# Kernel tuning notes

Hardware: AMD Instinct MI355X
Metric: run time of the kernel (lower is better)

The kernel has to match this reference:

```python
import jax, jax.numpy as jnp
import numpy as np
from jax import lax

B, L, D = 4, 2048, 1024
M = D // 4            # StructuredStateRecurrence memory_dim = dim//4
E, TOPK = 4, 2        # EnhancedGatedFusion defaults
H = D // 4            # LowRankFF hidden = dim//reduction_factor(4)
K, DIL = 5, 1         # SerriformBlock kernel_size=5, dilation init arg
EPS = 1e-6


def _rms(v, w):
    return w * v * lax.rsqrt(jnp.mean(v * v, axis=-1, keepdims=True) + EPS)


def setup_inputs() -> dict:
    key = jax.random.key(0)
    ks = jax.random.split(key, 16)
    g = lambda i, shape, s=0.02: jax.random.normal(ks[i], shape, jnp.float32) * s
    return {
        "x": jax.random.normal(ks[0], (B, L, D), jnp.float32),
        "memory_state": jnp.zeros((B, M), jnp.float32),
        "norm_w": jnp.ones((D,), jnp.float32),
        "dw_w": g(1, (D, K), 0.1),            # depthwise Conv1d weight [D,1,K] squeezed
        "dw_b": jnp.zeros((D,), jnp.float32),
        "pw_w": g(2, (D, D)),                 # pointwise Conv1d weight [D,D,1] squeezed
        "pw_b": jnp.zeros((D,), jnp.float32),
        "val_w": g(3, (M, D)),
        "val_b": jnp.zeros((M,), jnp.float32),
        "time_decay": g(4, (M,), 0.01),
        "time_first": g(5, (M,), 0.01),
        "gate_w": g(6, (D, D + M)),
        "gate_b": jnp.zeros((D,), jnp.float32),
        "router_w": g(7, (E, D)),
        "router_b": jnp.zeros((E,), jnp.float32),
        "exp_w": g(8, (E, D, D)),             # per-expert Linear(dim,dim) weights [out,in]
        "exp_b": jnp.zeros((E, D), jnp.float32),
        "out_w": g(9, (D, D)),
        "out_b": jnp.zeros((D,), jnp.float32),
        "fnorm_w": jnp.ones((D,), jnp.float32),
        "down_w": g(10, (H, D)),
        "down_b": jnp.zeros((H,), jnp.float32),
        "up_w": g(11, (D, H)),
        "up_b": jnp.zeros((D,), jnp.float32),
        "res_scale": jnp.array([0.9], jnp.float32),
    }


def reference(x, memory_state, norm_w, dw_w, dw_b, pw_w, pw_b, val_w, val_b,
              time_decay, time_first, gate_w, gate_b, router_w, router_b,
              exp_w, exp_b, out_w, out_b, fnorm_w, down_w, down_b, up_w,
              up_b, res_scale):
    h = _rms(x, norm_w)

    # --- FusedDWPWConv: causal depthwise conv + pointwise conv + SiLU ---
    pad = (K - 1) * DIL                                      # left causal pad (torch pads both, slices [:L])
    xc = jnp.swapaxes(h, 1, 2)                               # [B, D, L]
    y = lax.conv_general_dilated(xc, dw_w[:, None, :], (1,), [(pad, 0)],
                                 rhs_dilation=(DIL,),
                                 dimension_numbers=("NCL", "OIL", "NCL"),
                                 feature_group_count=D)
    y = y + dw_b[None, :, None]
    y = jax.nn.silu(jnp.einsum("oi,bil->bol", pw_w, y) + pw_b[None, :, None])
    h = jnp.swapaxes(y, 1, 2)                                # [B, L, D]

    # --- StructuredStateRecurrence: w[i] = decay*w[i-1] + v[i] (== torch's decay-mask sum) ---
    v = h @ val_w.T + val_b                                  # [B, L, M]
    decay = jax.nn.sigmoid(time_decay) * 0.9 + 0.1
    tfirst = jax.nn.sigmoid(time_first)

    def step(carry, v_t):
        w = carry * decay + v_t
        return w, w

    _, wv = lax.scan(step, jnp.zeros((x.shape[0], M), x.dtype), jnp.swapaxes(v, 0, 1))
    wv = jnp.swapaxes(wv, 0, 1)                              # [B, L, M]
    wv = wv + memory_state[:, None, :] * tfirst
    next_mem = wv[:, -1]
    h = h + jnp.concatenate([h, wv], axis=-1) @ gate_w.T + gate_b

    # --- EnhancedGatedFusion: top-k MoE over 4 experts ---
    logits = h @ router_w.T + router_b                       # [B, L, E]
    tk_logits, tk_idx = lax.top_k(logits, TOPK)
    tk_w = jax.nn.softmax(tk_logits, axis=-1)
    gates = jnp.sum(tk_w[..., None] * jax.nn.one_hot(tk_idx, E, dtype=h.dtype), axis=-2)  # [B,L,E]
    exp_out = jax.nn.silu(jnp.einsum("bli,eoi->bleo", h, exp_w) + exp_b)  # [B,L,E,D]
    comb = jnp.einsum("ble,bled->bld", gates, exp_out)
    h = _rms(h + comb @ out_w.T + out_b, fnorm_w)

    # --- LowRankFF (exact GELU, as torch nn.GELU default) ---
    ff = jax.nn.gelu(h @ down_w.T + down_b, approximate=False) @ up_w.T + up_b

    out = x * res_scale + (h + ff)
    return out, next_mem
```

## Files before the change

### kernel.cpp

```cpp
#include <hip/hip_runtime.h>
#include <hip/hip_bf16.h>
#include <math.h>

using bf16 = __hip_bfloat16;
typedef __attribute__((ext_vector_type(8))) short bfx8;
typedef __attribute__((ext_vector_type(4))) float fx4;

#define DI __device__ __forceinline__

#define B_  4
#define L_  2048
#define D_  1024
#define M_  256
#define N_  8192
#define H_  256
#define CCH 32
#define TCH 64

DI float us2f(unsigned short u){ unsigned int i=((unsigned int)u)<<16; float f; __builtin_memcpy(&f,&i,4); return f; }
DI unsigned short f2bu(float f){ bf16 h=__float2bfloat16(f); unsigned short u; __builtin_memcpy(&u,&h,2); return u; }
DI float b2f(bf16 v){ return __bfloat162float(v); }
DI float siluf(float x){ return x/(1.f+expf(-x)); }
DI float geluf(float x){ return 0.5f*x*(1.f+erff(x*0.70710678118654752f)); }

DI void gload_lds16(const bf16* g, bf16* l){
  __builtin_amdgcn_global_load_lds((const __attribute__((address_space(1))) void*)g,
                                   (__attribute__((address_space(3))) void*)l, 16, 0, 0);
}

__global__ __launch_bounds__(256) void k_prep(const float* __restrict__ pw_w, const float* __restrict__ val_w,
    const float* __restrict__ gate_w, const float* __restrict__ exp_w, const float* __restrict__ out_w,
    const float* __restrict__ down_w, const float* __restrict__ up_w,
    bf16* pwh, bf16* pwl, bf16* valh, bf16* vall, bf16* gatebf, bf16* expb, bf16* outb, bf16* downb, bf16* upb)
{
  for (int i = blockIdx.x*256 + threadIdx.x; i < 2097152; i += gridDim.x*256){
    const float* src; bf16* dsth; bf16* dstl = nullptr; int off;
    if (i < 262144)      { src=pw_w;   dsth=pwh;    dstl=pwl;  off=i; }
    else if (i < 327680) { src=val_w;  dsth=valh;   dstl=vall; off=i-262144; }
    else if (i < 655360) { src=gate_w; dsth=gatebf;            off=i-327680; }
    else if (i < 1703936){ src=exp_w;  dsth=expb;              off=i-655360; }
    else if (i < 1966080){ src=out_w;  dsth=outb;              off=i-1703936; }
    else if (i < 2031616){ src=down_w; dsth=downb;             off=i-1966080; }
    else                 { src=up_w;   dsth=upb;               off=i-2031616; }
    const float4 f = ((const float4*)src)[off];
    ushort4 h; h.x=f2bu(f.x); h.y=f2bu(f.y); h.z=f2bu(f.z); h.w=f2bu(f.w);
    ((ushort4*)dsth)[off] = h;
    if (dstl){
      ushort4 l;
      l.x=f2bu(f.x-us2f(h.x)); l.y=f2bu(f.y-us2f(h.y));
      l.z=f2bu(f.z-us2f(h.z)); l.w=f2bu(f.w-us2f(h.w));
      ((ushort4*)dstl)[off] = l;
    }
  }
}

__global__ __launch_bounds__(256) void k_precomp1(const float* __restrict__ rw, const float* __restrict__ gw,
                                                  float* __restrict__ part)
{
  const int bid = blockIdx.x;
  const int oc = bid/20, kb = bid - oc*20;
  const int ek = kb*256 + threadIdx.x;
  const int e = ek/1280, k = ek - e*1280;
  const float* rwe = rw + e*1024 + oc*128;
  const float* g   = gw + (size_t)(oc*128)*1280 + k;
  float acc = 0.f;
  #pragma unroll 8
  for (int o=0;o<128;o++) acc = fmaf(rwe[o], g[(size_t)o*1280], acc);
  part[oc*5120 + ek] = acc;
}

__global__ __launch_bounds__(256) void k_precomp2(const float* __restrict__ part, const float* __restrict__ rw,
                                                  const float* __restrict__ gb, const float* __restrict__ rb,
                                                  float* __restrict__ R, float* __restrict__ c0)
{
  const int ek = blockIdx.x*256 + threadIdx.x;
  if (ek < 5120){
    float s = 0.f;
    #pragma unroll
    for (int oc=0;oc<8;oc++) s += part[oc*5120 + ek];
    const int e = ek/1280, k = ek - e*1280;
    if (k < 1024) s += rw[e*1024 + k];
    R[ek] = s;
  } else if (ek < 5124){
    const int e = ek - 5120;
    float acc = rb[e];
    const float* rwe = rw + e*1024;
    #pragma unroll 8
    for (int o=0;o<1024;o++) acc = fmaf(rwe[o], gb[o], acc);
    c0[e] = acc;
  }
}

template<bool BF_OUT2>
__global__ __launch_bounds__(256) void k_rms(const float* inp, const float* __restrict__ w,
                                             float* outf, bf16* __restrict__ outbf)
{
  const int n = blockIdx.x, t = threadIdx.x;
  const float4 f = *((const float4*)inp + (size_t)n*(D_/4) + t);
  float s = f.x*f.x+f.y*f.y+f.z*f.z+f.w*f.w;
  #pragma unroll
  for (int off=32; off; off>>=1) s += __shfl_xor(s, off, 64);
  __shared__ float red[4];
  if ((t&63)==0) red[t>>6]=s;
  __syncthreads();
  const float inv = 1.f/sqrtf((red[0]+red[1]+red[2]+red[3])*(1.f/(float)D_)+1e-6f);
  const float4 wv = *((const float4*)w + t);
  float4 of;
  of.x = wv.x*f.x*inv; of.y = wv.y*f.y*inv; of.z = wv.z*f.z*inv; of.w = wv.w*f.w*inv;
  *((float4*)outf + (size_t)n*(D_/4) + t) = of;
  if constexpr (BF_OUT2){
    ushort4 ub; ub.x=f2bu(of.x); ub.y=f2bu(of.y); ub.z=f2bu(of.z); ub.w=f2bu(of.w);
    *((ushort4*)outbf + (size_t)n*(D_/4) + t) = ub;
  }
}

__global__ __launch_bounds__(256) void k_conv(const float* __restrict__ h0, const float* __restrict__ dww,
                                              const float* __restrict__ dwb,
                                              bf16* __restrict__ yhi, bf16* __restrict__ ylo)
{
  const int n = blockIdx.x, t = threadIdx.x;
  const int l = n & (L_-1);
  const int d0 = t*4;
  float a0=dwb[d0+0], a1=dwb[d0+1], a2=dwb[d0+2], a3=dwb[d0+3];
  #pragma unroll
  for (int k=0;k<5;k++){
    if (l-4+k < 0) continue;
    const float4 h4 = *(const float4*)&h0[(size_t)(n+k-4)*D_ + d0];
    a0 += h4.x*dww[(d0+0)*5+k];
    a1 += h4.y*dww[(d0+1)*5+k];
    a2 += h4.z*dww[(d0+2)*5+k];
    a3 += h4.w*dww[(d0+3)*5+k];
  }
  ushort4 hi, lo;
  hi.x=f2bu(a0); lo.x=f2bu(a0-us2f(hi.x));
  hi.y=f2bu(a1); lo.y=f2bu(a1-us2f(hi.y));
  hi.z=f2bu(a2); lo.z=f2bu(a2-us2f(hi.z));
  hi.w=f2bu(a3); lo.w=f2bu(a3-us2f(hi.w));
  *((ushort4*)yhi + (size_t)n*(D_/4) + t) = hi;
  *((ushort4*)ylo + (size_t)n*(D_/4) + t) = lo;
}

__global__ __launch_bounds__(256) void k_scan1(float* vw, float* __restrict__ carry,
                                               const float* __restrict__ td, const float* __restrict__ vb)
{
  const int bc = blockIdx.x, m = threadIdx.x;
  const int b = bc>>5, c = bc&(CCH-1);
  const float decay = 0.9f/(1.f+expf(-td[m])) + 0.1f;
  const float bias = vb[m];
  float* wp = vw + ((size_t)b*L_ + c*TCH)*M_ + m;
  float a = 0.f;
  for (int i=0;i<TCH;i++){ a = a*decay + (wp[(size_t)i*M_] + bias); wp[(size_t)i*M_] = a; }
  carry[(size_t)bc*M_ + m] = a;
}

__global__ void k_scan2(float* __restrict__ carry, const float* __restrict__ td)
{
  const int b = blockIdx.x, m = threadIdx.x;
  const float decay = 0.9f/(1.f+expf(-td[m])) + 0.1f;
  const float dT = powf(decay, (float)TCH);
  float cin = 0.f;
  for (int c=0;c<CCH;c++){
    const size_t idx = ((size_t)(b*CCH+c))*M_ + m;
    const float e = carry[idx];
    carry[idx] = cin;
    cin = e + dT*cin;
  }
}

__global__ __launch_bounds__(256) void k_scan3(const float* __restrict__ wv, const float* __restrict__ carry,
                                               const float* __restrict__ mem, const float* __restrict__ td,
                                               const float* __restrict__ tf,
                                               bf16* __restrict__ wvhi, bf16* __restrict__ wvlo,
                                               float* __restrict__ nextmem)
{
  const int bc = blockIdx.x, m = threadIdx.x;
  const int b = bc>>5, c = bc&(CCH-1);
  const float decay = 0.9f/(1.f+expf(-td[m])) + 0.1f;
  const float cin = carry[(size_t)bc*M_ + m];
  const float memc = mem[b*M_+m] / (1.f+expf(-tf[m]));
  const float* wp = wv + ((size_t)b*L_ + c*TCH)*M_ + m;
  float p = 1.f;
  for (int i=0;i<TCH;i++){
    p *= decay;
    const float val = wp[(size_t)i*M_] + p*cin + memc;
    const int l = c*TCH+i;
    const size_t n = (size_t)b*L_ + l;
    const unsigned short h = f2bu(val);
    wvhi[n*M_ + m] = *(const bf16*)&h;
    const unsigned short lo = f2bu(val - us2f(h));
    wvlo[n*M_ + m] = *(const bf16*)&lo;
    if (l == L_-1) nextmem[b*M_+m] = val;
  }
}

__global__ __launch_bounds__(256) void k_rgemv(const bf16* __restrict__ h1hi, const bf16* __restrict__ h1lo,
                                               const bf16* __restrict__ wvhi, const bf16* __restrict__ wvlo,
                                               const float* __restrict__ R, const float* __restrict__ c0,
                                               float* __restrict__ gates)
{
  const int wave = threadIdx.x>>6, lane = threadIdx.x&63;
  const size_t n = (size_t)blockIdx.x*4 + wave;
  float p0=0,p1=0,p2=0,p3=0;
  const ushort4* hhi = (const ushort4*)(h1hi + n*D_);
  const ushort4* hlo = (const ushort4*)(h1lo + n*D_);
  #pragma unroll
  for (int c=0;c<4;c++){
    const int k4 = c*64 + lane;
    const ushort4 uh = hhi[k4], ul = hlo[k4];
    const float v0=us2f(uh.x)+us2f(ul.x), v1=us2f(uh.y)+us2f(ul.y);
    const float v2=us2f(uh.z)+us2f(ul.z), v3=us2f(uh.w)+us2f(ul.w);
    const float4 r0 = *(const float4*)&R[0*1280 + k4*4];
    const float4 r1 = *(const float4*)&R[1*1280 + k4*4];
    const float4 r2 = *(const float4*)&R[2*1280 + k4*4];
    const float4 r3 = *(const float4*)&R[3*1280 + k4*4];
    p0 += v0*r0.x+v1*r0.y+v2*r0.z+v3*r0.w;
    p1 += v0*r1.x+v1*r1.y+v2*r1.z+v3*r1.w;
    p2 += v0*r2.x+v1*r2.y+v2*r2.z+v3*r2.w;
    p3 += v0*r3.x+v1*r3.y+v2*r3.z+v3*r3.w;
  }
  {
    const ushort4 uh = ((const ushort4*)(wvhi + n*M_))[lane];
    const ushort4 ul = ((const ushort4*)(wvlo + n*M_))[lane];
    const float v0=us2f(uh.x)+us2f(ul.x), v1=us2f(uh.y)+us2f(ul.y);
    const float v2=us2f(uh.z)+us2f(ul.z), v3=us2f(uh.w)+us2f(ul.w);
    const float4 r0 = *(const float4*)&R[0*1280 + 1024 + lane*4];
    const float4 r1 = *(const float4*)&R[1*1280 + 1024 + lane*4];
    const float4 r2 = *(const float4*)&R[2*1280 + 1024 + lane*4];
    const float4 r3 = *(const float4*)&R[3*1280 + 1024 + lane*4];
    p0 += v0*r0.x+v1*r0.y+v2*r0.z+v3*r0.w;
    p1 += v0*r1.x+v1*r1.y+v2*r1.z+v3*r1.w;
    p2 += v0*r2.x+v1*r2.y+v2*r2.z+v3*r2.w;
    p3 += v0*r3.x+v1*r3.y+v2*r3.z+v3*r3.w;
  }
  #pragma unroll
  for (int off=32; off; off>>=1){
    p0 += __shfl_xor(p0, off, 64); p1 += __shfl_xor(p1, off, 64);
    p2 += __shfl_xor(p2, off, 64); p3 += __shfl_xor(p3, off, 64);
  }
  if (lane==0){
    float lg[4] = {p0+c0[0], p1+c0[1], p2+c0[2], p3+c0[3]};
    int i1=0; float m1=lg[0];
    #pragma unroll
    for (int e=1;e<4;e++) if (lg[e]>m1){ m1=lg[e]; i1=e; }
    int i2=-1; float m2=-1e30f;
    #pragma unroll
    for (int e=0;e<4;e++) if (e!=i1 && lg[e]>m2){ m2=lg[e]; i2=e; }
    const float ex = expf(m2-m1);
    const float w1 = 1.f/(1.f+ex), w2 = ex/(1.f+ex);
    float4 g; g.x=0; g.y=0; g.z=0; g.w=0;
    ((float*)&g)[i1]=w1; ((float*)&g)[i2]=w2;
    *(float4*)&gates[n*4] = g;
  }
}

__global__ __launch_bounds__(256) void k_count(const float* __restrict__ gates, int* __restrict__ cnt)
{
  const int n = blockIdx.x*256 + threadIdx.x;
  const float4 g = *(const float4*)&gates[(size_t)n*4];
  if (g.x>0.f) atomicAdd(&cnt[0],1);
  if (g.y>0.f) atomicAdd(&cnt[1],1);
  if (g.z>0.f) atomicAdd(&cnt[2],1);
  if (g.w>0.f) atomicAdd(&cnt[3],1);
}

__global__ void k_base(const int* __restrict__ cnt, int* __restrict__ base, int* __restrict__ cnt2)
{
  if (threadIdx.x==0){
    int s=0;
    for (int e=0;e<4;e++){ base[e]=s; s += ((cnt[e]+127)>>7)<<7; }
    base[4]=s; base[5]=s>>7;
    for (int e=0;e<4;e++) cnt2[e]=0;
  }
}

__global__ __launch_bounds__(256) void k_assign(const float* __restrict__ gates, const int* __restrict__ base,
                                                int* __restrict__ cnt2, unsigned int* __restrict__ midx,
                                                float* __restrict__ mw)
{
  const int n = blockIdx.x*256 + threadIdx.x;
  const int lane = threadIdx.x & 63;
  const float4 g = *(const float4*)&gates[(size_t)n*4];
  const float ga[4] = {g.x,g.y,g.z,g.w};
  int ea=-1, ebx=-1; float wa=0.f, wb=0.f;
  #pragma unroll
  for (int e=0;e<4;e++){
    const float ge = ga[e];
    if (ge>0.f){ if (ea<0){ea=e;wa=ge;} else {ebx=e;wb=ge;} }
  }
  int s0e, s1e=-1; float s0w, s1w=0.f;
  if (ebx<0){ s0e=ea; s0w=wa; }
  else if (wa>=wb){ s0e=ea; s0w=wa; s1e=ebx; s1w=wb; }
  else            { s0e=ebx; s0w=wb; s1e=ea; s1w=wa; }

  #pragma unroll
  for (int e=0;e<4;e++){
    #pragma unroll
    for (int slot=0;slot<2;slot++){
      const bool want = (slot==0) ? (s0e==e) : (s1e==e);
      const unsigned long long mask = __ballot(want);
      if (mask == 0ull) continue;
      const int leader = __ffsll((long long)mask) - 1;
      int pos = 0;
      if (lane == leader) pos = atomicAdd(&cnt2[e], __popcll(mask));
      pos = __shfl(pos, leader, 64);
      if (want){
        const int rank = __popcll(mask & ((1ull<<lane)-1ull));
        const int idx = base[e] + pos + rank;
        midx[idx] = (unsigned)n | (slot ? 0x80000000u : 0u);
        mw[idx]   = slot ? s1w : s0w;
      }
    }
  }
}

__global__ __launch_bounds__(256) void k_expa(const bf16* __restrict__ A, const bf16* __restrict__ Wall,
                                              const float* __restrict__ eb,
                                              const unsigned int* __restrict__ midx, const float* __restrict__ mw,
                                              const int* __restrict__ base, const int* __restrict__ cnt,
                                              bf16* __restrict__ S0, bf16* __restrict__ S1)
{
  __shared__ __align__(16) bf16 smem[8192];
  bf16* Ash = smem;
  bf16* Wsh = smem + 4096;

  const int bid = blockIdx.x;
  const int id2 = (bid&7)*132 + (bid>>3);
  const int rblk = id2>>3, bcol0 = (id2&7)<<7;
  if (rblk >= base[5]) return;
  const int row0 = rblk<<7;
  int e=0;
  if (row0 >= base[1]) e=1;
  if (row0 >= base[2]) e=2;
  if (row0 >= base[3]) e=3;
  const int loc0 = row0 - base[e];
  const int cnte = cnt[e];

  const int t = threadIdx.x, wave = t>>6, lane = t&63;
  const int wm = wave>>1, wn = wave&1;
  fx4 acc[4][4] = {};

  const int sr = t>>2;
  const int sc = ((t&3) ^ ((t>>3)&3))*8;
  const unsigned mr0 = midx[row0+sr], mr1 = midx[row0+64+sr];
  const int tok0 = min((int)(mr0 & 0x7FFFFFFFu), N_-1);
  const int tok1 = min((int)(mr1 & 0x7FFFFFFFu), N_-1);
  const bf16* gA0 = A + (size_t)tok0*D_ + sc;
  const bf16* gA1 = A + (size_t)tok1*D_ + sc;
  const bf16* gW0 = Wall + (size_t)e*D_*D_ + (size_t)(bcol0+sr)*D_ + sc;
  const bf16* gW1 = gW0 + (size_t)64*D_;

  bf16* dA = Ash + wave*512;
  bf16* dW = Wsh + wave*512;
  const int koff = ((lane>>4) ^ ((lane>>1)&3))*8;
  const int aoff = (wm*64 + (lane&15))*32 + koff;
  const int boff = (wn*64 + (lane&15))*32 + koff;

  for (int kk=0; kk<D_; kk+=32){
    __syncthreads();
    gload_lds16(gA0 + kk, dA);
    gload_lds16(gA1 + kk, dA + 2048);
    gload_lds16(gW0 + kk, dW);
    gload_lds16(gW1 + kk, dW + 2048);
    __syncthreads();
    bfx8 ah[4], wh[4];
    #pragma unroll
    for (int i=0;i<4;i++){
      ah[i] = *(const bfx8*)&Ash[aoff + i*512];
      wh[i] = *(const bfx8*)&Wsh[boff + i*512];
    }
    #pragma unroll
    for (int i=0;i<4;i++)
      #pragma unroll
      for (int j=0;j<4;j++)
        acc[i][j] = __builtin_amdgcn_mfma_f32_16x16x32_bf16(ah[i], wh[j], acc[i][j], 0,0,0);
  }

  const int r0l = wm*64 + (lane>>4)*4;
  const int c0l = wn*64 + (lane&15);
  #pragma unroll
  for (int i=0;i<4;i++){
    #pragma unroll
    for (int r=0;r<4;r++){
      const int loc = loc0 + r0l + i*16 + r;
      if (loc >= cnte) continue;
      const int gr = row0 + r0l + i*16 + r;
      const unsigned mi = midx[gr];
      const int tok = (int)(mi & 0x7FFFFFFFu);
      const float w = mw[gr];
      bf16* Sd = (mi & 0x80000000u) ? S1 : S0;
      #pragma unroll
      for (int j=0;j<4;j++){
        const int col = bcol0 + c0l + j*16;
        const float v = acc[i][j][r] + eb[(e<<10)+col];
        Sd[(size_t)tok*D_ + col] = __float2bfloat16(w*siluf(v));
      }
    }
  }
}

__global__ __launch_bounds__(256) void k_combine(const bf16* __restrict__ S0, const bf16* __restrict__ S1,
                                                 bf16* __restrict__ o, int n4)
{
  int i = blockIdx.x*256 + threadIdx.x;
  const int stride = gridDim.x*256;
  for (; i<n4; i+=stride){
    const ushort4 a = ((const ushort4*)S0)[i];
    const ushort4 b = ((const ushort4*)S1)[i];
    ushort4 c;
    c.x = f2bu(us2f(a.x)+us2f(b.x));
    c.y = f2bu(us2f(a.y)+us2f(b.y));
    c.z = f2bu(us2f(a.z)+us2f(b.z));
    c.w = f2bu(us2f(a.w)+us2f(b.w));
    ((ushort4*)o)[i] = c;
  }
}

enum GMode { MODE_PW=0, MODE_VAL, MODE_GATE, MODE_OUTW, MODE_DOWN, MODE_UP };

template<int MODE>
__global__ __launch_bounds__(256)
void k_gemm(const bf16* __restrict__ Ah, const bf16* __restrict__ Al, const int lda,
            const bf16* __restrict__ A2h,
            const bf16* __restrict__ Wh, const bf16* __restrict__ Wl, const int K,
            const float* __restrict__ bias,
            float* Cf, const int ldc,
            bf16* __restrict__ Cb1, bf16* __restrict__ Cb2, const int ldcb,
            const float* resf, const int ldres,
            const float* __restrict__ xin, const float* __restrict__ rs)
{
  constexpr bool SPLIT = (MODE==MODE_PW || MODE==MODE_VAL);
  constexpr bool DUAL  = (MODE==MODE_GATE);
  __shared__ __align__(16) bf16 smem[SPLIT ? 16384 : 8192];
  bf16* Ash = smem;
  bf16* Wsh = smem + 4096;
  bf16* Asl = smem + (SPLIT ? 8192 : 0);
  bf16* Wsl = smem + (SPLIT ? 12288 : 0);

  const int t = threadIdx.x, wave = t>>6, lane = t&63;
  const int bid = blockIdx.x;
  int brow, bcol, kz = 0;
  if constexpr (MODE==MODE_VAL){
    const int id2 = (bid&7)*64 + (bid>>3);
    const int ct = id2 & 7;
    bcol = (ct&1)<<7; kz = ct>>1; brow = (id2>>3)<<7;
  } else if constexpr (MODE==MODE_DOWN){
    const int id2 = (bid&7)*16 + (bid>>3);
    bcol = (id2&1)<<7; brow = (id2>>1)<<7;
  } else {
    const int id2 = (bid&7)*64 + (bid>>3);
    bcol = (id2&7)<<7; brow = (id2>>3)<<7;
  }
  const int wm = wave>>1, wn = wave&1;
  fx4 acc[4][4] = {};

  const int sr = t>>2;
  const int sc = ((t&3) ^ ((t>>3)&3))*8;
  const size_t rg = (size_t)(brow+sr);
  const bf16* gAh0 = Ah + rg*lda + sc;
  const bf16* gAh1 = gAh0 + (size_t)64*lda;
  const bf16* gAl0 = SPLIT ? Al + rg*lda + sc : nullptr;
  const bf16* gAl1 = SPLIT ? gAl0 + (size_t)64*lda : nullptr;
  const bf16* gWh0 = Wh + (size_t)(bcol+sr)*K + sc;
  const bf16* gWh1 = gWh0 + (size_t)64*K;
  const bf16* gWl0 = SPLIT ? Wl + (size_t)(bcol+sr)*K + sc : nullptr;
  const bf16* gWl1 = SPLIT ? gWl0 + (size_t)64*K : nullptr;
  const bf16* g2h0 = DUAL ? A2h + rg*M_ + sc : nullptr;
  const bf16* g2h1 = DUAL ? g2h0 + (size_t)64*M_ : nullptr;

  bf16* dA  = Ash + wave*512;
  bf16* dW  = Wsh + wave*512;
  bf16* dAl = Asl + wave*512;
  bf16* dWl = Wsl + wave*512;

  const int k0 = (MODE==MODE_VAL) ? (kz<<8) : 0;
  const int k1 = (MODE==MODE_VAL) ? (k0+256) : K;

  const int koff = ((lane>>4) ^ ((lane>>1)&3))*8;
  const int aoff = (wm*64 + (lane&15))*32 + koff;
  const int boff = (wn*64 + (lane&15))*32 + koff;

  for (int kk=k0; kk<k1; kk+=32){
    __syncthreads();
    if constexpr (DUAL){
      if (kk < 1024){
        gload_lds16(gAh0 + kk, dA);
        gload_lds16(gAh1 + kk, dA + 2048);
      } else {
        gload_lds16(g2h0 + (kk-1024), dA);
        gload_lds16(g2h1 + (kk-1024), dA + 2048);
      }
    } else {
      gload_lds16(gAh0 + kk, dA);
      gload_lds16(gAh1 + kk, dA + 2048);
      if constexpr (SPLIT){
        gload_lds16(gAl0 + kk, dAl);
        gload_lds16(gAl1 + kk, dAl + 2048);
      }
    }
    gload_lds16(gWh0 + kk, dW);
    gload_lds16(gWh1 + kk, dW + 2048);
    if constexpr (SPLIT){
      gload_lds16(gWl0 + kk, dWl);
      gload_lds16(gWl1 + kk, dWl + 2048);
    }
    __syncthreads();

    bfx8 ah[4], al[4], wh[4], wl[4];
    #pragma unroll
    for (int i=0;i<4;i++){
      ah[i] = *(const bfx8*)&Ash[aoff + i*512];
      wh[i] = *(const bfx8*)&Wsh[boff + i*512];
      if constexpr (SPLIT){
        al[i] = *(const bfx8*)&Asl[aoff + i*512];
        wl[i] = *(const bfx8*)&Wsl[boff + i*512];
      }
    }
    #pragma unroll
    for (int i=0;i<4;i++){
      #pragma unroll
      for (int j=0;j<4;j++){
        acc[i][j] = __builtin_amdgcn_mfma_f32_16x16x32_bf16(ah[i], wh[j], acc[i][j], 0,0,0);
        if constexpr (SPLIT){
          acc[i][j] = __builtin_amdgcn_mfma_f32_16x16x32_bf16(al[i], wh[j], acc[i][j], 0,0,0);
          acc[i][j] = __builtin_amdgcn_mfma_f32_16x16x32_bf16(ah[i], wl[j], acc[i][j], 0,0,0);
        }
      }
    }
  }

  const int r0 = brow + wm*64 + (lane>>4)*4;
  const int c0 = bcol + wn*64 + (lane&15);
  #pragma unroll
  for (int j=0;j<4;j++){
    const int col = c0 + j*16;
    float bc = 0.f;
    if constexpr (MODE!=MODE_VAL) bc = bias[col];
    #pragma unroll
    for (int i=0;i<4;i++){
      #pragma unroll
      for (int r=0;r<4;r++){
        const size_t rr = (size_t)(r0 + i*16 + r);
        float v = acc[i][j][r] + bc;
        if constexpr (MODE==MODE_PW){
          v = siluf(v);
          const unsigned short h = f2bu(v);
          Cb1[rr*ldcb+col] = *(const bf16*)&h;
          const unsigned short lo = f2bu(v - us2f(h));
          Cb2[rr*ldcb+col] = *(const bf16*)&lo;
        } else if constexpr (MODE==MODE_VAL){
          atomicAdd(&Cf[rr*ldc+col], v);
        } else if constexpr (MODE==MODE_GATE){
          v += b2f(Ah[rr*(size_t)lda+col]) + b2f(Al[rr*(size_t)lda+col]);
          Cf[rr*ldc+col] = v;
          Cb1[rr*ldcb+col] = __float2bfloat16(v);
        } else if constexpr (MODE==MODE_OUTW){
          Cf[rr*ldc+col] = v + resf[rr*ldres+col];
        } else if constexpr (MODE==MODE_DOWN){
          Cb1[rr*ldcb+col] = __float2bfloat16(geluf(v));
        } else if constexpr (MODE==MODE_UP){
          Cf[rr*ldc+col] = xin[rr*D_+col]*rs[0] + resf[rr*ldres+col] + v;
        }
      }
    }
  }
}

extern "C" void kernel_launch(void* const* d_in, const int* in_sizes, int n_in,
                              void* d_out, int out_size, void* d_ws, size_t ws_size,
                              hipStream_t stream)
{
  (void)in_sizes; (void)n_in; (void)out_size; (void)ws_size;
  const float* x       = (const float*)d_in[0];
  const float* mem     = (const float*)d_in[1];
  const float* norm_w  = (const float*)d_in[2];
  const float* dw_w    = (const float*)d_in[3];
  const float* dw_b    = (const float*)d_in[4];
  const float* pw_w    = (const float*)d_in[5];
  const float* pw_b    = (const float*)d_in[6];
  const float* val_w   = (const float*)d_in[7];
  const float* val_b   = (const float*)d_in[8];
  const float* td      = (const float*)d_in[9];
  const float* tf      = (const float*)d_in[10];
  const float* gate_w  = (const float*)d_in[11];
  const float* gate_b  = (const float*)d_in[12];
  const float* rw      = (const float*)d_in[13];
  const float* rb      = (const float*)d_in[14];
  const float* exp_w   = (const float*)d_in[15];
  const float* exp_b   = (const float*)d_in[16];
  const float* out_w   = (const float*)d_in[17];
  const float* out_b   = (const float*)d_in[18];
  const float* fnorm_w = (const float*)d_in[19];
  const float* down_w  = (const float*)d_in[20];
  const float* down_b  = (const float*)d_in[21];
  const float* up_w    = (const float*)d_in[22];
  const float* up_b    = (const float*)d_in[23];
  const float* rs      = (const float*)d_in[24];

  char* ws = (char*)d_ws;
  const size_t MB = 1048576;
  bf16* pwh    = (bf16*)(ws + 0);
  bf16* pwl    = (bf16*)(ws + 2*MB);
  bf16* valh   = (bf16*)(ws + 4*MB);
  bf16* vall   = (bf16*)(ws + 4*MB + 524288);
  bf16* gatebf = (bf16*)(ws + 5*MB);
  bf16* expb   = (bf16*)(ws + 7*MB + 524288);
  bf16* outb   = (bf16*)(ws + 15*MB + 524288);
  bf16* downb  = (bf16*)(ws + 17*MB + 524288);
  bf16* upb    = (bf16*)(ws + 18*MB);
  float* gatesb= (float*)(ws + 18*MB + 524288);
  float* Rbuf  = (float*)(ws + 18*MB + 655360);
  float* c0buf = (float*)(ws + 18*MB + 655360 + 20480);
  float* carry = (float*)(ws + 18*MB + 786432);
  char* MZ = ws + 18*MB + 917504;
  int*   cntb  = (int*)(MZ);
  int*   cnt2b = (int*)(MZ + 64);
  int*   baseb = (int*)(MZ + 128);
  unsigned int* midx = (unsigned int*)(MZ + 4096);
  float* mwb   = (float*)(MZ + 4096 + 69632);
  float* partb = (float*)(ws + 19*MB + 209715);
  float* h0    = (float*)(ws + 20*MB);
  float* vbuf  = (float*)(ws + 20*MB);
  float* h2    = (float*)(ws + 20*MB);
  bf16*  h3bf  = (bf16 *)(ws + 20*MB);
  bf16*  dbf   = (bf16 *)(ws + 36*MB);
  bf16*  yhi   = (bf16 *)(ws + 52*MB);
  bf16*  ylo   = (bf16 *)(ws + 68*MB);
  bf16*  h2bf  = (bf16 *)(ws + 52*MB);
  bf16*  wvhi  = (bf16 *)(ws + 68*MB);
  bf16*  wvlo  = (bf16 *)(ws + 72*MB);
  bf16*  S0    = (bf16 *)(ws + 68*MB);
  bf16*  h1hi  = (bf16 *)(ws + 84*MB);
  bf16*  h1lo  = (bf16 *)(ws + 100*MB);
  bf16*  S1    = (bf16 *)(ws + 84*MB);
  bf16*  combbf= (bf16 *)(ws + 100*MB);

  float* out0 = (float*)d_out;
  float* nm   = (float*)d_out + (size_t)N_*D_;
  float* tbuf = (float*)d_out;
  float* h3   = (float*)d_out;

  const dim3 blk(256);
  k_prep<<<1024, blk, 0, stream>>>(pw_w, val_w, gate_w, exp_w, out_w, down_w, up_w,
                                   pwh, pwl, valh, vall, gatebf, expb, outb, downb, upb);
  k_precomp1<<<160, blk, 0, stream>>>(rw, gate_w, partb);
  k_precomp2<<<21, blk, 0, stream>>>(partb, rw, gate_b, rb, Rbuf, c0buf);
  (void)hipMemsetAsync(MZ, 0, 256, stream);
  k_rms<false><<<N_, blk, 0, stream>>>(x, norm_w, h0, nullptr);
  k_conv<<<N_, blk, 0, stream>>>(h0, dw_w, dw_b, yhi, ylo);
  k_gemm<MODE_PW><<<512, blk, 0, stream>>>(yhi, ylo, D_, nullptr, pwh, pwl, D_,
      pw_b, nullptr, 0, h1hi, h1lo, D_, nullptr, 0, nullptr, nullptr);
  (void)hipMemsetAsync(vbuf, 0, (size_t)N_*M_*4, stream);
  k_gemm<MODE_VAL><<<512, blk, 0, stream>>>(h1hi, h1lo, D_, nullptr, valh, vall, D_,
      nullptr, vbuf, M_, nullptr, nullptr, 0, nullptr, 0, nullptr, nullptr);
  k_scan1<<<B_*CCH, blk, 0, stream>>>(vbuf, carry, td, val_b);
  k_scan2<<<B_, blk, 0, stream>>>(carry, td);
  k_scan3<<<B_*CCH, blk, 0, stream>>>(vbuf, carry, mem, td, tf, wvhi, wvlo, nm);
  k_gemm<MODE_GATE><<<512, blk, 0, stream>>>(h1hi, h1lo, D_, wvhi, gatebf, nullptr, 1280,
      gate_b, h2, D_, h2bf, nullptr, D_, nullptr, 0, nullptr, nullptr);
  k_rgemv<<<N_/4, blk, 0, stream>>>(h1hi, h1lo, wvhi, wvlo, Rbuf, c0buf, gatesb);
  k_count<<<N_/256, blk, 0, stream>>>(gatesb, cntb);
  k_base<<<1, 64, 0, stream>>>(cntb, baseb, cnt2b);
  k_assign<<<N_/256, blk, 0, stream>>>(gatesb, baseb, cnt2b, midx, mwb);
  (void)hipMemsetAsync(S1, 0, (size_t)N_*D_*2, stream);
  k_expa<<<1056, blk, 0, stream>>>(h2bf, expb, exp_b, midx, mwb, baseb, cntb, S0, S1);
  k_combine<<<2048, blk, 0, stream>>>(S0, S1, combbf, N_*D_/4);
  k_gemm<MODE_OUTW><<<512, blk, 0, stream>>>(combbf, nullptr, D_, nullptr, outb, nullptr, D_,
      out_b, tbuf, D_, nullptr, nullptr, 0, h2, D_, nullptr, nullptr);
  k_rms<true><<<N_, blk, 0, stream>>>(tbuf, fnorm_w, h3, h3bf);
  k_gemm<MODE_DOWN><<<128, blk, 0, stream>>>(h3bf, nullptr, D_, nullptr, downb, nullptr, D_,
      down_b, nullptr, 0, dbf, nullptr, H_, nullptr, 0, nullptr, nullptr);
  k_gemm<MODE_UP><<<512, blk, 0, stream>>>(dbf, nullptr, H_, nullptr, upb, nullptr, H_,
      up_b, out0, D_, nullptr, nullptr, 0, h3, D_, x, rs);
}
```

Before: 522.4 us.

## Double-buffer LDS tiles in expert and dense GEMM kernels

Splits the K-loop of the expert GEMM and the templated dense GEMM into stage and compute steps over two LDS buffers. The next tile's global-to-LDS loads are issued before the MFMAs on the current tile, so each iteration needs one barrier instead of two. This aims to hide global load latency behind matrix math, at the cost of doubling shared memory per block (up to 64KB for the split-precision modes), which may reduce occupancy.

```diff
diff --git a/kernel.cpp b/kernel.cpp
--- a/kernel.cpp
+++ b/kernel.cpp
@@ -319,9 +319,7 @@
                                               const int* __restrict__ base, const int* __restrict__ cnt,
                                               bf16* __restrict__ S0, bf16* __restrict__ S1)
 {
-  __shared__ __align__(16) bf16 smem[8192];
-  bf16* Ash = smem;
-  bf16* Wsh = smem + 4096;
+  __shared__ __align__(16) bf16 smem[2*8192];
 
   const int bid = blockIdx.x;
   const int id2 = (bid&7)*132 + (bid>>3);
@@ -349,19 +347,21 @@
   const bf16* gW0 = Wall + (size_t)e*D_*D_ + (size_t)(bcol0+sr)*D_ + sc;
   const bf16* gW1 = gW0 + (size_t)64*D_;
 
-  bf16* dA = Ash + wave*512;
-  bf16* dW = Wsh + wave*512;
   const int koff = ((lane>>4) ^ ((lane>>1)&3))*8;
   const int aoff = (wm*64 + (lane&15))*32 + koff;
   const int boff = (wn*64 + (lane&15))*32 + koff;
 
-  for (int kk=0; kk<D_; kk+=32){
-    __syncthreads();
+  auto stage = [&](int kk, int buf){
+    bf16* dA = smem + buf*8192 + wave*512;
+    bf16* dW = smem + buf*8192 + 4096 + wave*512;
     gload_lds16(gA0 + kk, dA);
     gload_lds16(gA1 + kk, dA + 2048);
     gload_lds16(gW0 + kk, dW);
     gload_lds16(gW1 + kk, dW + 2048);
-    __syncthreads();
+  };
+  auto compute = [&](int buf){
+    const bf16* Ash = smem + buf*8192;
+    const bf16* Wsh = Ash + 4096;
     bfx8 ah[4], wh[4];
     #pragma unroll
     for (int i=0;i<4;i++){
@@ -373,7 +373,18 @@
       #pragma unroll
       for (int j=0;j<4;j++)
         acc[i][j] = __builtin_amdgcn_mfma_f32_16x16x32_bf16(ah[i], wh[j], acc[i][j], 0,0,0);
-  }
+  };
+
+  stage(0, 0);
+  __syncthreads();
+  int cur = 0;
+  for (int kk=32; kk<D_; kk+=32){
+    stage(kk, cur^1);
+    compute(cur);
+    __syncthreads();
+    cur ^= 1;
+  }
+  compute(cur);
 
   const int r0l = wm*64 + (lane>>4)*4;
   const int c0l = wn*64 + (lane&15);
@@ -430,11 +441,8 @@
 {
   constexpr bool SPLIT = (MODE==MODE_PW || MODE==MODE_VAL);
   constexpr bool DUAL  = (MODE==MODE_GATE);
-  __shared__ __align__(16) bf16 smem[SPLIT ? 16384 : 8192];
-  bf16* Ash = smem;
-  bf16* Wsh = smem + 4096;
-  bf16* Asl = smem + (SPLIT ? 8192 : 0);
-  bf16* Wsl = smem + (SPLIT ? 12288 : 0);
+  constexpr int  BUFS  = SPLIT ? 16384 : 8192;
+  __shared__ __align__(16) bf16 smem[2*BUFS];
 
   const int t = threadIdx.x, wave = t>>6, lane = t&63;
   const int bid = blockIdx.x;
@@ -467,11 +475,6 @@
   const bf16* g2h0 = DUAL ? A2h + rg*M_ + sc : nullptr;
   const bf16* g2h1 = DUAL ? g2h0 + (size_t)64*M_ : nullptr;
 
-  bf16* dA  = Ash + wave*512;
-  bf16* dW  = Wsh + wave*512;
-  bf16* dAl = Asl + wave*512;
-  bf16* dWl = Wsl + wave*512;
-
   const int k0 = (MODE==MODE_VAL) ? (kz<<8) : 0;
   const int k1 = (MODE==MODE_VAL) ? (k0+256) : K;
 
@@ -479,8 +482,9 @@
   const int aoff = (wm*64 + (lane&15))*32 + koff;
   const int boff = (wn*64 + (lane&15))*32 + koff;
 
-  for (int kk=k0; kk<k1; kk+=32){
-    __syncthreads();
+  auto stage = [&](int kk, int buf){
+    bf16* dA = smem + buf*BUFS + wave*512;
+    bf16* dW = smem + buf*BUFS + 4096 + wave*512;
     if constexpr (DUAL){
       if (kk < 1024){
         gload_lds16(gAh0 + kk, dA);
@@ -493,6 +497,7 @@
       gload_lds16(gAh0 + kk, dA);
       gload_lds16(gAh1 + kk, dA + 2048);
       if constexpr (SPLIT){
+        bf16* dAl = smem + buf*BUFS + 8192 + wave*512;
         gload_lds16(gAl0 + kk, dAl);
         gload_lds16(gAl1 + kk, dAl + 2048);
       }
@@ -500,19 +505,22 @@
     gload_lds16(gWh0 + kk, dW);
     gload_lds16(gWh1 + kk, dW + 2048);
     if constexpr (SPLIT){
+      bf16* dWl = smem + buf*BUFS + 12288 + wave*512;
       gload_lds16(gWl0 + kk, dWl);
       gload_lds16(gWl1 + kk, dWl + 2048);
     }
-    __syncthreads();
-
+  };
+  auto compute = [&](int buf){
+    const bf16* Ash = smem + buf*BUFS;
+    const bf16* Wsh = Ash + 4096;
     bfx8 ah[4], al[4], wh[4], wl[4];
     #pragma unroll
     for (int i=0;i<4;i++){
       ah[i] = *(const bfx8*)&Ash[aoff + i*512];
       wh[i] = *(const bfx8*)&Wsh[boff + i*512];
       if constexpr (SPLIT){
-        al[i] = *(const bfx8*)&Asl[aoff + i*512];
-        wl[i] = *(const bfx8*)&Wsl[boff + i*512];
+        al[i] = *(const bfx8*)&Ash[8192 + aoff + i*512];
+        wl[i] = *(const bfx8*)&Ash[12288 + boff + i*512];
       }
     }
     #pragma unroll
@@ -526,7 +534,18 @@
         }
       }
     }
-  }
+  };
+
+  stage(k0, 0);
+  __syncthreads();
+  int cur = 0;
+  for (int kk=k0+32; kk<k1; kk+=32){
+    stage(kk, cur^1);
+    compute(cur);
+    __syncthreads();
+    cur ^= 1;
+  }
+  compute(cur);
 
   const int r0 = brow + wm*64 + (lane>>4)*4;
   const int c0 = bcol + wn*64 + (lane&15);
```

Result: no change. 512.6 us (-1.9%).
